# Kernel optimization log

Measured on AMD Instinct MI355X. Metric: run time of the kernel, lower is better.

The kernel has to match this reference:

```python
import jax, jax.numpy as jnp
import numpy as np

ALPHA = 0.2
WINDOW = 5
LAYER_CNN = 3
LAYER_OUT = 3
BIDAT = 4
B, N, M, CD, GD, NH, LD, PD = 32, 128, 1024, 128, 64, 4, 256, 40


def _gat(h, adj, W, a, concat):
    # e[b,i,j] = leaky_relu(a1 . Wh_i + a2 . Wh_j)  (decomposed repeat_interleave+cat+matmul)
    Wh = jnp.einsum('bnf,fg->bng', h, W)
    g = W.shape[1]
    e = jax.nn.leaky_relu(jnp.einsum('bng,g->bn', Wh, a[:g, 0])[:, :, None]
                          + jnp.einsum('bng,g->bn', Wh, a[g:, 0])[:, None, :], ALPHA)
    e = jnp.where(adj > 0, e, jnp.float32(-9e15))
    att = jax.nn.softmax(e, axis=2)
    hp = jnp.einsum('bnm,bmg->bng', att, Wh)
    return jax.nn.elu(hp) if concat else hp


def _mask_softmax(a, mask):
    a_exp = jnp.exp(a - jnp.max(a, -1, keepdims=True)) * mask
    return a_exp / (jnp.sum(a_exp, -1, keepdims=True) + 1e-6)


def reference(atoms_emb, adjacency, atoms_mask, amino_emb, amino_mask, fps, inv_Temp, Temp,
              bert_W, bert_b, gat_W, gat_a, gatout_W, gatout_a, Wcomp_W, Wcomp_b,
              prot_W, prot_b, conv_W, conv_b, Wprot_W, Wprot_b,
              U, tc2p_W, tc2p_b, tp2c_W, tp2c_b, bhc_W, bhc_b, bhp_W, bhp_b,
              battc_W, battc_b, battp_W, battp_b, combc_W, combc_b, combp_W, combp_b,
              Wout_W, Wout_b, out_W, out_b):
    # compound branch: bert projection 300 -> comp_dim, then multi-head GAT
    h = jnp.einsum('bnc,cd->bnd', atoms_emb, bert_W) + bert_b
    heads = jax.vmap(lambda W, a: _gat(h, adjacency, W, a, True))(gat_W, gat_a)  # [H,B,N,GD]
    multi = jnp.moveaxis(heads, 0, 2).reshape(h.shape[0], h.shape[1], -1)        # [B,N,H*GD]
    av = jax.nn.elu(_gat(multi, adjacency, gatout_W, gatout_a, False))
    av = jax.nn.leaky_relu(jnp.einsum('bnd,dl->bnl', av, Wcomp_W) + Wcomp_b, ALPHA)  # [B,N,LD]
    # protein branch: 1024 -> prot_dim, stacked 2D conv (1 channel), prot_dim -> latent
    pv = jnp.einsum('bmc,cd->bmd', amino_emb, prot_W) + prot_b  # [B,M,PD]
    x = pv[:, None, :, :]  # NCHW
    for i in range(LAYER_CNN):
        x = jax.nn.leaky_relu(
            jax.lax.conv_general_dilated(x, conv_W[i][None, None], (1, 1),
                                         [(WINDOW, WINDOW), (WINDOW, WINDOW)],
                                         dimension_numbers=('NCHW', 'OIHW', 'NCHW')) + conv_b[i], ALPHA)
    pv = jax.nn.leaky_relu(jnp.einsum('bmd,dl->bml', x[:, 0], Wprot_W) + Wprot_b, ALPHA)  # [B,M,LD]
    # bidirectional U-bilinear co-attention, BIDAT rounds
    cfs, pfs = [], []
    for i in range(BIDAT):
        A = jnp.tanh(jnp.einsum('bnl,lk,bmk->bnm', av, U[i], pv))
        A = A * atoms_mask[:, :, None] * amino_mask[:, None, :]
        atoms_trans = jnp.einsum('bnm,bml->bnl', A, jnp.tanh(jnp.einsum('bml,lk->bmk', pv, tp2c_W[i]) + tp2c_b[i]))
        amino_trans = jnp.einsum('bnm,bnl->bml', A, jnp.tanh(jnp.einsum('bnl,lk->bnk', av, tc2p_W[i]) + tc2p_b[i]))
        atoms_tmp = jnp.concatenate([jnp.tanh(jnp.einsum('bnl,lk->bnk', av, bhc_W[i]) + bhc_b[i]), atoms_trans], -1)
        amino_tmp = jnp.concatenate([jnp.tanh(jnp.einsum('bml,lk->bmk', pv, bhp_W[i]) + bhp_b[i]), amino_trans], -1)
        atoms_att = _mask_softmax(jnp.einsum('bnd,d->bn', atoms_tmp, battc_W[i]) + battc_b[i], atoms_mask)
        amino_att = _mask_softmax(jnp.einsum('bmd,d->bm', amino_tmp, battp_W[i]) + battp_b[i], amino_mask)
        cfs.append(jnp.sum(av * atoms_att[:, :, None], 1))
        pfs.append(jnp.sum(pv * amino_att[:, :, None], 1))
    cat_cf = jnp.concatenate(cfs, 1)  # [B, BIDAT*LD]
    cat_pf = jnp.concatenate(pfs, 1)
    cf_final = jnp.concatenate([cat_cf @ combc_W + combc_b, fps], 1)
    pf_final = cat_pf @ combp_W + combp_b
    v = jnp.concatenate([cf_final, pf_final, inv_Temp, Temp], 1)  # [B, 3*LD+2]
    for j in range(LAYER_OUT):
        v = jax.nn.leaky_relu(v @ Wout_W[j] + Wout_b[j], ALPHA)
    return v @ out_W + out_b  # [B,1]


def setup_inputs():
    ks = jax.random.split(jax.random.key(0), 64)
    def nrm(i, shape, s=0.1):
        return (jax.random.normal(ks[i], shape) * s).astype(jnp.float32)
    adjacency = jax.random.randint(ks[0], (B, N, N), 0, 2).astype(jnp.int32)
    adjacency = jnp.maximum(adjacency, jnp.eye(N, dtype=jnp.int32)[None])  # self-loops
    K = 2 * WINDOW + 1
    return dict(
        atoms_emb=nrm(1, (B, N, 300), 1.0),
        adjacency=adjacency,
        atoms_mask=jnp.ones((B, N), jnp.float32),
        amino_emb=nrm(2, (B, M, 1024), 1.0),
        amino_mask=jnp.ones((B, M), jnp.float32),
        fps=nrm(3, (B, LD), 1.0),
        inv_Temp=jax.random.uniform(ks[4], (B, 1), jnp.float32),
        Temp=jax.random.uniform(ks[5], (B, 1), jnp.float32),
        bert_W=nrm(6, (300, CD)), bert_b=nrm(7, (CD,)),
        gat_W=nrm(8, (NH, CD, GD)), gat_a=nrm(9, (NH, 2 * GD, 1)),
        gatout_W=nrm(10, (NH * GD, CD)), gatout_a=nrm(11, (2 * CD, 1)),
        Wcomp_W=nrm(12, (CD, LD)), Wcomp_b=nrm(13, (LD,)),
        prot_W=nrm(14, (1024, PD)), prot_b=nrm(15, (PD,)),
        conv_W=nrm(16, (LAYER_CNN, K, K)), conv_b=nrm(17, (LAYER_CNN,)),
        Wprot_W=nrm(18, (PD, LD)), Wprot_b=nrm(19, (LD,)),
        U=nrm(20, (BIDAT, LD, LD)),
        tc2p_W=nrm(21, (BIDAT, LD, LD)), tc2p_b=nrm(22, (BIDAT, LD)),
        tp2c_W=nrm(23, (BIDAT, LD, LD)), tp2c_b=nrm(24, (BIDAT, LD)),
        bhc_W=nrm(25, (BIDAT, LD, LD)), bhc_b=nrm(26, (BIDAT, LD)),
        bhp_W=nrm(27, (BIDAT, LD, LD)), bhp_b=nrm(28, (BIDAT, LD)),
        battc_W=nrm(29, (BIDAT, 2 * LD)), battc_b=nrm(30, (BIDAT,)),
        battp_W=nrm(31, (BIDAT, 2 * LD)), battp_b=nrm(32, (BIDAT,)),
        combc_W=nrm(33, (BIDAT * LD, LD)), combc_b=nrm(34, (LD,)),
        combp_W=nrm(35, (BIDAT * LD, LD)), combp_b=nrm(36, (LD,)),
        Wout_W=nrm(37, (LAYER_OUT, 3 * LD + 2, 3 * LD + 2)), Wout_b=nrm(38, (LAYER_OUT, 3 * LD + 2)),
        out_W=nrm(39, (3 * LD + 2, 1)), out_b=nrm(40, (1,)),
    )
```

## Files before the change

kernel.cpp:

```cpp
#include <hip/hip_runtime.h>
#include <math.h>

#define ALPHA_LR 0.2f

#define Bq  32
#define Nq  128
#define Mq  1024
#define CDq 128
#define GDq 64
#define NHq 4
#define LDq 256
#define PDq 40

typedef unsigned short ushort_t;
typedef __attribute__((ext_vector_type(8))) short bf16x8;
typedef __attribute__((ext_vector_type(4))) float f32x4;

__device__ __forceinline__ ushort_t f2bf(float f) {
    union { float f; unsigned u; } x; x.f = f;
    unsigned r = x.u + 0x7FFFu + ((x.u >> 16) & 1u);
    return (ushort_t)(r >> 16);
}
__device__ __forceinline__ float bf2f(ushort_t u) {
    union { unsigned u; float f; } x; x.u = ((unsigned)u) << 16;
    return x.f;
}
__device__ __forceinline__ float ftanh(float x) {
    float e = __expf(2.f * x);
    return 1.f - 2.f * __builtin_amdgcn_rcpf(e + 1.f);
}

template<int ACT, int MASKED, int HAS_BIAS, int NT, int AF32, int OUTBF>
__global__ __launch_bounds__(256) void mfma_nt_k(
    int M, int N, int K, int Nout,
    const void* __restrict__ Av, int lda, long long sA,
    const ushort_t* __restrict__ Bt, int ldb, long long sB,
    const float* __restrict__ bias, long long sBias,
    void* __restrict__ Cv, int ldc, long long sC,
    const float* __restrict__ maskR, long long sW2,
    const float* __restrict__ maskC)
{
    int z = blockIdx.z;
    Bt += (long long)z * sB;
    if (HAS_BIAS) bias += (long long)z * sBias;
    float* C = nullptr; ushort_t* Cb = nullptr;
    if (OUTBF) Cb = (ushort_t*)Cv + (long long)z * sC;
    else       C  = (float*)Cv + (long long)z * sC;

    int wave = threadIdx.x >> 6;
    int lane = threadIdx.x & 63;
    int lr = lane & 15;
    int kg = lane >> 4;
    int m0 = (blockIdx.x * 4 + wave) * 16;
    int n0 = blockIdx.y * (NT * 16);
    if (m0 >= M) return;

    f32x4 acc[NT];
    #pragma unroll
    for (int t = 0; t < NT; t++) acc[t] = (f32x4){0.f, 0.f, 0.f, 0.f};

    const ushort_t* Ab = nullptr;
    const float*    Af = nullptr;
    if (AF32) Af = (const float*)Av + (long long)z * sA + (long long)(m0 + lr) * lda + kg * 8;
    else      Ab = (const ushort_t*)Av + (long long)z * sA + (long long)(m0 + lr) * lda + kg * 8;
    const ushort_t* Bbase = Bt + (long long)(n0 + lr) * ldb + kg * 8;

    for (int k0 = 0; k0 < K; k0 += 32) {
        bf16x8 a;
        if (AF32) {
            float4 a0 = *(const float4*)(Af + k0);
            float4 a1 = *(const float4*)(Af + k0 + 4);
            a[0] = (short)f2bf(a0.x); a[1] = (short)f2bf(a0.y);
            a[2] = (short)f2bf(a0.z); a[3] = (short)f2bf(a0.w);
            a[4] = (short)f2bf(a1.x); a[5] = (short)f2bf(a1.y);
            a[6] = (short)f2bf(a1.z); a[7] = (short)f2bf(a1.w);
        } else {
            a = *(const bf16x8*)(Ab + k0);
        }
        #pragma unroll
        for (int t = 0; t < NT; t++) {
            bf16x8 b = *(const bf16x8*)(Bbase + (long long)t * 16 * ldb + k0);
            acc[t] = __builtin_amdgcn_mfma_f32_16x16x32_bf16(a, b, acc[t], 0, 0, 0);
        }
    }

    int row0 = m0 + kg * 4;
    #pragma unroll
    for (int t = 0; t < NT; t++) {
        int col = n0 + t * 16 + lr;
        if (col >= Nout) continue;
        float bv = HAS_BIAS ? bias[col] : 0.f;
        float mC = MASKED ? maskC[(long long)z * N + col] : 1.f;
        #pragma unroll
        for (int r = 0; r < 4; r++) {
            float v = acc[t][r] + bv;
            if (ACT == 1) v = v > 0.f ? v : ALPHA_LR * v;
            else if (ACT == 2) v = ftanh(v);
            if (MASKED) v *= maskR[(long long)z * M + row0 + r] * mC;
            if (OUTBF) Cb[(long long)(row0 + r) * ldc + col] = f2bf(v);
            else       C[(long long)(row0 + r) * ldc + col] = v;
        }
    }
}

__global__ __launch_bounds__(256) void pv0_k(
    const float* __restrict__ amino,
    const ushort_t* __restrict__ Bt,
    const float* __restrict__ bias,
    float* __restrict__ C)
{
    __shared__ float As[64][68];
    int tid = threadIdx.x;
    int wave = tid >> 6, lane = tid & 63;
    int lr = lane & 15, kg = lane >> 4;
    int m0 = blockIdx.x * 64;

    f32x4 acc[3];
    #pragma unroll
    for (int t = 0; t < 3; t++) acc[t] = (f32x4){0.f, 0.f, 0.f, 0.f};

    int srow = tid >> 2;
    int scol = (tid & 3) * 16;
    const float* srcbase = amino + (long long)(m0 + srow) * 1024 + scol;

    for (int k0 = 0; k0 < 1024; k0 += 64) {
        float4 v0 = *(const float4*)(srcbase + k0);
        float4 v1 = *(const float4*)(srcbase + k0 + 4);
        float4 v2 = *(const float4*)(srcbase + k0 + 8);
        float4 v3 = *(const float4*)(srcbase + k0 + 12);
        *(float4*)&As[srow][scol]      = v0;
        *(float4*)&As[srow][scol + 4]  = v1;
        *(float4*)&As[srow][scol + 8]  = v2;
        *(float4*)&As[srow][scol + 12] = v3;
        __syncthreads();
        #pragma unroll
        for (int ks = 0; ks < 2; ks++) {
            const float* ap = &As[wave * 16 + lr][ks * 32 + kg * 8];
            bf16x8 a;
            #pragma unroll
            for (int j = 0; j < 8; j++) a[j] = (short)f2bf(ap[j]);
            #pragma unroll
            for (int t = 0; t < 3; t++) {
                bf16x8 bfr = *(const bf16x8*)(Bt + (long long)(t * 16 + lr) * 1024 + k0 + ks * 32 + kg * 8);
                acc[t] = __builtin_amdgcn_mfma_f32_16x16x32_bf16(a, bfr, acc[t], 0, 0, 0);
            }
        }
        __syncthreads();
    }
    int row0 = m0 + wave * 16 + kg * 4;
    #pragma unroll
    for (int t = 0; t < 3; t++) {
        int col = t * 16 + lr;
        if (col >= PDq) continue;
        float bv = bias[col];
        #pragma unroll
        for (int r = 0; r < 4; r++)
            C[(long long)(row0 + r) * PDq + col] = acc[t][r] + bv;
    }
}

__global__ __launch_bounds__(256) void mfma_reduceF_k(
    int M,
    const ushort_t* __restrict__ A,
    const ushort_t* __restrict__ W8,
    const float* __restrict__ bias8,
    const float* __restrict__ w28,
    float* __restrict__ C)
{
    int z = blockIdx.z;
    const ushort_t* W = W8 + (long long)z * 65536;
    const float* bias = bias8 + z * 256;
    const float* w2   = w28 + z * 256;
    float* Cz = C + (long long)z * M;

    __shared__ ushort_t Bs[64 * 256];

    int tid = threadIdx.x;
    int wave = tid >> 6, lane = tid & 63;
    int lr = lane & 15, kg = lane >> 4;
    int m0 = blockIdx.x * 128 + wave * 16;

    const ushort_t* Ab0 = A + (long long)(m0 + lr) * 256 + kg * 8;
    const ushort_t* Ab1 = Ab0 + 64 * 256;
    bf16x8 areg0[8], areg1[8];
    #pragma unroll
    for (int kb = 0; kb < 8; kb++) {
        areg0[kb] = *(const bf16x8*)(Ab0 + kb * 32);
        areg1[kb] = *(const bf16x8*)(Ab1 + kb * 32);
    }

    float rs0[4] = {0.f, 0.f, 0.f, 0.f};
    float rs1[4] = {0.f, 0.f, 0.f, 0.f};

    for (int ph = 0; ph < 4; ph++) {
        int n0 = ph * 64;
        #pragma unroll
        for (int step = 0; step < 8; step++) {
            int g = step * 256 + tid;
            int row = g >> 5, slot = g & 31;
            uint4 v = *(const uint4*)(W + (long long)(n0 + row) * 256 + slot * 8);
            int dst = row * 512 + ((slot * 16) ^ ((row & 31) << 4));
            *(uint4*)((char*)Bs + dst) = v;
        }
        __syncthreads();

        {
            f32x4 acc[4];
            #pragma unroll
            for (int t = 0; t < 4; t++) acc[t] = (f32x4){0.f, 0.f, 0.f, 0.f};
            #pragma unroll
            for (int kb = 0; kb < 8; kb++) {
                #pragma unroll
                for (int t = 0; t < 4; t++) {
                    int rowl = t * 16 + lr;
                    int colb = (kg * 16 + kb * 64) ^ ((rowl & 31) << 4);
                    bf16x8 b = *(const bf16x8*)((char*)Bs + rowl * 512 + colb);
                    acc[t] = __builtin_amdgcn_mfma_f32_16x16x32_bf16(areg0[kb], b, acc[t], 0, 0, 0);
                }
            }
            #pragma unroll
            for (int t = 0; t < 4; t++) {
                int col = n0 + t * 16 + lr;
                float bv = bias[col], wv = w2[col];
                #pragma unroll
                for (int r = 0; r < 4; r++)
                    rs0[r] += ftanh(acc[t][r] + bv) * wv;
            }
        }
        {
            f32x4 acc[4];
            #pragma unroll
            for (int t = 0; t < 4; t++) acc[t] = (f32x4){0.f, 0.f, 0.f, 0.f};
            #pragma unroll
            for (int kb = 0; kb < 8; kb++) {
                #pragma unroll
                for (int t = 0; t < 4; t++) {
                    int rowl = t * 16 + lr;
                    int colb = (kg * 16 + kb * 64) ^ ((rowl & 31) << 4);
                    bf16x8 b = *(const bf16x8*)((char*)Bs + rowl * 512 + colb);
                    acc[t] = __builtin_amdgcn_mfma_f32_16x16x32_bf16(areg1[kb], b, acc[t], 0, 0, 0);
                }
            }
            #pragma unroll
            for (int t = 0; t < 4; t++) {
                int col = n0 + t * 16 + lr;
                float bv = bias[col], wv = w2[col];
                #pragma unroll
                for (int r = 0; r < 4; r++)
                    rs1[r] += ftanh(acc[t][r] + bv) * wv;
            }
        }
        __syncthreads();
    }

    #pragma unroll
    for (int r = 0; r < 4; r++) {
        rs0[r] += __shfl_xor(rs0[r], 1, 64);
        rs0[r] += __shfl_xor(rs0[r], 2, 64);
        rs0[r] += __shfl_xor(rs0[r], 4, 64);
        rs0[r] += __shfl_xor(rs0[r], 8, 64);
        rs1[r] += __shfl_xor(rs1[r], 1, 64);
        rs1[r] += __shfl_xor(rs1[r], 2, 64);
        rs1[r] += __shfl_xor(rs1[r], 4, 64);
        rs1[r] += __shfl_xor(rs1[r], 8, 64);
    }
    if (lr == 0) {
        int row0 = m0 + kg * 4;
        #pragma unroll
        for (int r = 0; r < 4; r++) {
            Cz[row0 + r] = rs0[r];
            Cz[row0 + 64 + r] = rs1[r];
        }
    }
}

__global__ __launch_bounds__(256) void pack8_k(
    const float* __restrict__ b1, const float* __restrict__ b2,
    const float* __restrict__ w1, int w1Off,
    const float* __restrict__ w2v, int w2Off,
    float* __restrict__ bias8, float* __restrict__ w28)
{
    int j = blockIdx.x * 256 + threadIdx.x;
    int slot = j >> 8, c = j & 255;
    bias8[j] = slot < 4 ? b1[slot * 256 + c] : b2[(slot - 4) * 256 + c];
    w28[j]   = slot < 4 ? w1[slot * 512 + w1Off + c] : w2v[(slot - 4) * 512 + w2Off + c];
}

__global__ __launch_bounds__(256) void bidat_fused_k(
    const ushort_t* __restrict__ avU_all,
    const ushort_t* __restrict__ pv_bf,
    const float* __restrict__ rbuf_all,
    const float* __restrict__ qbuf_all,
    const float* __restrict__ atoms_mask,
    const float* __restrict__ amino_mask,
    float* __restrict__ scoreCp,
    float* __restrict__ csump)
{
    int z = blockIdx.z;
    int i = z >> 5, b = z & 31;
    int gx = blockIdx.x;
    int gy = blockIdx.y;
    int wave = threadIdx.x >> 6;
    int lane = threadIdx.x & 63;
    int lr = lane & 15, kg = lane >> 4;

    int n0 = gx * 64 + wave * 16;
    const ushort_t* Ab = avU_all + ((long long)i * 4096 + (long long)b * 128 + n0 + lr) * 256 + kg * 8;
    bf16x8 areg[8];
    #pragma unroll
    for (int kb = 0; kb < 8; kb++) areg[kb] = *(const bf16x8*)(Ab + kb * 32);

    const float* rI = rbuf_all + (long long)i * 32768 + (long long)b * 1024;
    const float* qI = qbuf_all + (long long)i * 4096 + (long long)b * 128;
    const float* mR = atoms_mask + (long long)b * 128;
    const float* mC = amino_mask + (long long)b * 1024;

    float mRn[4], qn[4];
    #pragma unroll
    for (int r = 0; r < 4; r++) {
        int n = n0 + kg * 4 + r;
        mRn[r] = mR[n];
        qn[r]  = qI[n];
    }

    float sc[4] = {0.f, 0.f, 0.f, 0.f};
    __shared__ float cl[4][64];

    for (int mt = 0; mt < 4; mt++) {
        int m0 = (gy * 4 + mt) * 64;
        const ushort_t* Bb = pv_bf + ((long long)b * 1024 + m0 + lr) * 256 + kg * 8;

        f32x4 acc[4];
        #pragma unroll
        for (int t = 0; t < 4; t++) acc[t] = (f32x4){0.f, 0.f, 0.f, 0.f};
        #pragma unroll
        for (int kb = 0; kb < 8; kb++) {
            #pragma unroll
            for (int t = 0; t < 4; t++) {
                bf16x8 bfr = *(const bf16x8*)(Bb + (long long)t * 16 * 256 + kb * 32);
                acc[t] = __builtin_amdgcn_mfma_f32_16x16x32_bf16(areg[kb], bfr, acc[t], 0, 0, 0);
            }
        }

        float cs[4] = {0.f, 0.f, 0.f, 0.f};
        #pragma unroll
        for (int t = 0; t < 4; t++) {
            int m = m0 + t * 16 + lr;
            float mc = mC[m];
            float rv = rI[m];
            #pragma unroll
            for (int r = 0; r < 4; r++) {
                float a = ftanh(acc[t][r]) * mRn[r] * mc;
                sc[r] += a * rv;
                cs[t] += a * qn[r];
            }
        }
        #pragma unroll
        for (int t = 0; t < 4; t++) {
            cs[t] += __shfl_xor(cs[t], 16, 64);
            cs[t] += __shfl_xor(cs[t], 32, 64);
        }
        __syncthreads();
        if (kg == 0) {
            #pragma unroll
            for (int t = 0; t < 4; t++) cl[wave][t * 16 + lr] = cs[t];
        }
        __syncthreads();
        if (threadIdx.x < 64) {
            float s = cl[0][threadIdx.x] + cl[1][threadIdx.x]
                    + cl[2][threadIdx.x] + cl[3][threadIdx.x];
            csump[((long long)z * 2 + gx) * 1024 + m0 + threadIdx.x] = s;
        }
    }

    #pragma unroll
    for (int r = 0; r < 4; r++) {
        sc[r] += __shfl_xor(sc[r], 1, 64);
        sc[r] += __shfl_xor(sc[r], 2, 64);
        sc[r] += __shfl_xor(sc[r], 4, 64);
        sc[r] += __shfl_xor(sc[r], 8, 64);
    }
    if (lr == 0) {
        #pragma unroll
        for (int r = 0; r < 4; r++) {
            int n = gx * 64 + wave * 16 + kg * 4 + r;
            scoreCp[((long long)z * 4 + gy) * 128 + n] = sc[r];
        }
    }
}

__global__ __launch_bounds__(128) void finishC_sm_k(
    const float* __restrict__ scoreCp, const float* __restrict__ hbdot_all,
    const float* __restrict__ battc_b, const float* __restrict__ mask,
    float* __restrict__ scoreC_all)
{
    int z = blockIdx.x;
    int i = z >> 5, b = z & 31;
    int n = threadIdx.x;
    __shared__ float red[128];
    float s = 0.f;
    #pragma unroll
    for (int gy = 0; gy < 4; gy++)
        s += scoreCp[((long long)z * 4 + gy) * 128 + n];
    s += hbdot_all[(long long)i * 4096 + b * 128 + n] + battc_b[i];
    red[n] = s; __syncthreads();
    for (int off = 64; off > 0; off >>= 1) {
        if (n < off) red[n] = fmaxf(red[n], red[n + off]);
        __syncthreads();
    }
    float mx = red[0];
    __syncthreads();
    float e = __expf(s - mx) * mask[(long long)b * 128 + n];
    red[n] = e; __syncthreads();
    for (int off = 64; off > 0; off >>= 1) {
        if (n < off) red[n] += red[n + off];
        __syncthreads();
    }
    float inv = 1.0f / (red[0] + 1e-6f);
    scoreC_all[(long long)z * 128 + n] = e * inv;
}

__global__ __launch_bounds__(256) void finishP_sm_k(
    const float* __restrict__ csump, const float* __restrict__ hpbdot_all,
    const float* __restrict__ battp_b, const float* __restrict__ mask,
    float* __restrict__ scoreP_all)
{
    int z = blockIdx.x;
    int i = z >> 5, b = z & 31;
    int t = threadIdx.x;
    __shared__ float red[256];
    float vals[4];
    float mx = -1e30f;
    #pragma unroll
    for (int j = 0; j < 4; j++) {
        int m = j * 256 + t;
        float s = csump[((long long)z * 2 + 0) * 1024 + m]
                + csump[((long long)z * 2 + 1) * 1024 + m]
                + hpbdot_all[(long long)i * 32768 + (long long)b * 1024 + m]
                + battp_b[i];
        vals[j] = s;
        mx = fmaxf(mx, s);
    }
    red[t] = mx; __syncthreads();
    for (int off = 128; off > 0; off >>= 1) {
        if (t < off) red[t] = fmaxf(red[t], red[t + off]);
        __syncthreads();
    }
    mx = red[0];
    __syncthreads();
    float sum = 0.f;
    #pragma unroll
    for (int j = 0; j < 4; j++) {
        float e = __expf(vals[j] - mx) * mask[(long long)b * 1024 + j * 256 + t];
        vals[j] = e; sum += e;
    }
    red[t] = sum; __syncthreads();
    for (int off = 128; off > 0; off >>= 1) {
        if (t < off) red[t] += red[t + off];
        __syncthreads();
    }
    float inv = 1.0f / (red[0] + 1e-6f);
    #pragma unroll
    for (int j = 0; j < 4; j++)
        scoreP_all[(long long)z * 1024 + j * 256 + t] = vals[j] * inv;
}

__global__ __launch_bounds__(256) void cvtpad_bf16_k(
    const float* __restrict__ in, ushort_t* __restrict__ out,
    int rows, int Ksrc, int Kdst)
{
    long long idx = (long long)blockIdx.x * 256 + threadIdx.x;
    long long total = (long long)rows * Kdst;
    if (idx >= total) return;
    int r = (int)(idx / Kdst), k = (int)(idx % Kdst);
    out[idx] = (k < Ksrc) ? f2bf(in[(long long)r * Ksrc + k]) : (ushort_t)0;
}

struct WtEnt {
    const float* W; ushort_t* Wt;
    int K, Nsrc, Npad, Kp, zcnt, blkStart;
};
struct WtTab { WtEnt e[11]; };

__global__ __launch_bounds__(256) void wtcvtAll_k(WtTab tab)
{
    int blk = blockIdx.x;
    int ei = 0;
    #pragma unroll
    for (int i = 1; i < 11; i++) if (blk >= tab.e[i].blkStart) ei = i;
    WtEnt E = tab.e[ei];
    long long perZ = (long long)E.Npad * E.Kp;
    long long lidx = (long long)(blk - E.blkStart) * 256 + threadIdx.x;
    if (lidx >= perZ * E.zcnt) return;
    int z = (int)(lidx / perZ);
    long long idx = lidx % perZ;
    int n = (int)(idx / E.Kp), k = (int)(idx % E.Kp);
    const float* Wz = E.W + (long long)z * E.K * E.Nsrc;
    ushort_t* Oz = E.Wt + (long long)z * perZ;
    float v = (k < E.K && n < E.Nsrc) ? Wz[(long long)k * E.Nsrc + n] : 0.f;
    Oz[idx] = f2bf(v);
}

__global__ __launch_bounds__(128) void gat_e_k(
    const float* __restrict__ Wh, int ldWh, int GD,
    const float* __restrict__ a, int aStride,
    float* __restrict__ esrc, float* __restrict__ edst, int rows)
{
    int row = blockIdx.x;
    int k = blockIdx.y;
    int g = threadIdx.x;
    float ws = 0.f, wd = 0.f;
    if (g < GD) {
        float wv = Wh[(long long)row * ldWh + k * GD + g];
        ws = wv * a[k * aStride + g];
        wd = wv * a[k * aStride + GD + g];
    }
    __shared__ float sb[2][128];
    sb[0][threadIdx.x] = ws; sb[1][threadIdx.x] = wd;
    __syncthreads();
    for (int off = 64; off > 0; off >>= 1) {
        if (threadIdx.x < off) {
            sb[0][threadIdx.x] += sb[0][threadIdx.x + off];
            sb[1][threadIdx.x] += sb[1][threadIdx.x + off];
        }
        __syncthreads();
    }
    if (threadIdx.x == 0) {
        esrc[(long long)k * rows + row] = sb[0][0];
        edst[(long long)k * rows + row] = sb[1][0];
    }
}

template<int GD>
__global__ __launch_bounds__(256) void gat_attn2_k(
    const float* __restrict__ Wh, int ldWh,
    const int* __restrict__ adj,
    const float* __restrict__ esrc, const float* __restrict__ edst,
    ushort_t* __restrict__ outp, int ldOut)
{
    int row = blockIdx.x;
    int k = blockIdx.y;
    int rows = gridDim.x;
    int b = row >> 7, n = row & 127;
    int tid = threadIdx.x;

    __shared__ float att[128];
    __shared__ float red[128];
    __shared__ float sred[256];

    if (tid < 128) {
        float e = esrc[(long long)k * rows + row] + edst[(long long)k * rows + b * 128 + tid];
        e = e > 0.f ? e : ALPHA_LR * e;
        if (adj[(long long)b * 16384 + n * 128 + tid] <= 0) e = -9.0e15f;
        att[tid] = e;
        red[tid] = e;
    }
    __syncthreads();
    for (int off = 64; off > 0; off >>= 1) {
        if (tid < off) red[tid] = fmaxf(red[tid], red[tid + off]);
        __syncthreads();
    }
    float mx = red[0];
    __syncthreads();
    if (tid < 128) {
        float ex = __expf(att[tid] - mx);
        att[tid] = ex;
        red[tid] = ex;
    }
    __syncthreads();
    for (int off = 64; off > 0; off >>= 1) {
        if (tid < off) red[tid] += red[tid + off];
        __syncthreads();
    }
    float inv = 1.0f / red[0];
    __syncthreads();

    constexpr int SPLIT = 256 / GD;
    constexpr int CH = 128 / SPLIT;
    int g = tid % GD;
    int part = tid / GD;
    const float* Whb = Wh + (long long)(b * 128) * ldWh + k * GD + g;
    float s = 0.f;
    int mm0 = part * CH;
    for (int mm = mm0; mm < mm0 + CH; mm++)
        s += att[mm] * Whb[(long long)mm * ldWh];
    sred[part * GD + g] = s;
    __syncthreads();
    if (part == 0) {
        float tot = s;
        #pragma unroll
        for (int p = 1; p < SPLIT; p++) tot += sred[p * GD + g];
        tot *= inv;
        tot = tot > 0.f ? tot : expm1f(tot);
        outp[(long long)row * ldOut + k * GD + g] = f2bf(tot);
    }
}

__global__ __launch_bounds__(256) void conv3_k(
    const float* __restrict__ x,
    const float* __restrict__ Wc,
    const float* __restrict__ bc,
    ushort_t* __restrict__ y)
{
    __shared__ float wsh[3][121];
    __shared__ float A[94][50];
    __shared__ float Bv[84][50];
    __shared__ float Cv[74][50];

    int tid = threadIdx.x;
    int b = blockIdx.y;
    int m0 = blockIdx.x * 64;

    for (int i = tid; i < 363; i += 256) wsh[i / 121][i % 121] = Wc[i];
    const float* xb = x + (long long)b * Mq * PDq;
    for (int idx = tid; idx < 94 * 50; idx += 256) {
        int row = idx / 50, col = idx % 50;
        int gm = m0 - 15 + row, d = col - 5;
        float v = 0.f;
        if (d >= 0 && d < PDq && gm >= 0 && gm < Mq)
            v = xb[(long long)gm * PDq + d];
        A[row][col] = v;
    }
    __syncthreads();

    {
        float b0 = bc[0];
        for (int idx = tid; idx < 84 * 50; idx += 256) {
            int row = idx / 50, col = idx % 50;
            float s = 0.f;
            if (col >= 5 && col < 45) {
                int d = col - 5;
                #pragma unroll
                for (int i = 0; i < 11; i++)
                    #pragma unroll
                    for (int j = 0; j < 11; j++)
                        s += A[row + i][d + j] * wsh[0][i * 11 + j];
                s += b0;
                s = s > 0.f ? s : ALPHA_LR * s;
            }
            Bv[row][col] = s;
        }
    }
    __syncthreads();

    {
        float b1 = bc[1];
        for (int idx = tid; idx < 74 * 50; idx += 256) {
            int row = idx / 50, col = idx % 50;
            float s = 0.f;
            if (col >= 5 && col < 45) {
                int d = col - 5;
                #pragma unroll
                for (int i = 0; i < 11; i++)
                    #pragma unroll
                    for (int j = 0; j < 11; j++)
                        s += Bv[row + i][d + j] * wsh[1][i * 11 + j];
                s += b1;
                s = s > 0.f ? s : ALPHA_LR * s;
            }
            Cv[row][col] = s;
        }
    }
    __syncthreads();

    {
        float b2 = bc[2];
        for (int idx = tid; idx < 64 * 64; idx += 256) {
            int row = idx / 64, d = idx % 64;
            long long o = ((long long)b * Mq + m0 + row) * 64 + d;
            if (d >= PDq) { y[o] = 0; continue; }
            float s = 0.f;
            #pragma unroll
            for (int i = 0; i < 11; i++)
                #pragma unroll
                for (int j = 0; j < 11; j++)
                    s += Cv[row + i][d + j] * wsh[2][i * 11 + j];
            s += b2;
            s = s > 0.f ? s : ALPHA_LR * s;
            y[o] = f2bf(s);
        }
    }
}

__global__ __launch_bounds__(256) void wsum1B4_k(
    const ushort_t* __restrict__ feat, const float* __restrict__ att_all,
    float* __restrict__ partial, int L)
{
    int b = blockIdx.x, c = blockIdx.y, l = threadIdx.x;
    int chunk = L / 16;
    const ushort_t* fb = feat + (long long)b * L * LDq;
    const float* a0 = att_all + ((long long)0 * Bq + b) * L;
    const float* a1 = att_all + ((long long)1 * Bq + b) * L;
    const float* a2 = att_all + ((long long)2 * Bq + b) * L;
    const float* a3 = att_all + ((long long)3 * Bq + b) * L;
    float s0 = 0.f, s1 = 0.f, s2 = 0.f, s3 = 0.f;
    int r0 = c * chunk, r1 = r0 + chunk;
    for (int r = r0; r < r1; r++) {
        float f = bf2f(fb[(long long)r * LDq + l]);
        s0 += f * a0[r]; s1 += f * a1[r];
        s2 += f * a2[r]; s3 += f * a3[r];
    }
    partial[(((long long)0 * Bq + b) * 16 + c) * LDq + l] = s0;
    partial[(((long long)1 * Bq + b) * 16 + c) * LDq + l] = s1;
    partial[(((long long)2 * Bq + b) * 16 + c) * LDq + l] = s2;
    partial[(((long long)3 * Bq + b) * 16 + c) * LDq + l] = s3;
}

__global__ __launch_bounds__(256) void wsum2B_k(
    const float* __restrict__ partial, float* __restrict__ out)
{
    int b = blockIdx.x, i = blockIdx.y, l = threadIdx.x;
    float s = 0.f;
    #pragma unroll
    for (int c = 0; c < 16; c++)
        s += partial[(((long long)i * Bq + b) * 16 + c) * LDq + l];
    out[(long long)b * 4 * LDq + i * LDq + l] = s;
}

template<int ACT>
__global__ __launch_bounds__(256) void headlin_k(
    const float* __restrict__ vin, int ldv, int VD,
    const float* __restrict__ W, int ldw,
    const float* __restrict__ bias,
    float* __restrict__ vout, int ldo, int OD, int colBase)
{
    int b = blockIdx.x;
    int c = threadIdx.x & 63;
    int s = threadIdx.x >> 6;
    int col = blockIdx.y * 64 + c;

    __shared__ float vs[1024];
    for (int i = threadIdx.x; i < VD; i += 256) vs[i] = vin[(long long)b * ldv + i];
    __syncthreads();

    float sum = 0.f;
    if (col < OD) {
        int k0 = (VD * s) >> 2, k1 = (VD * (s + 1)) >> 2;
        #pragma unroll 4
        for (int k = k0; k < k1; k++)
            sum += vs[k] * W[(long long)k * ldw + col];
    }
    __shared__ float red[4][64];
    red[s][c] = sum;
    __syncthreads();
    if (s == 0 && col < OD) {
        float t = red[0][c] + red[1][c] + red[2][c] + red[3][c] + bias[col];
        if (ACT == 1) t = t > 0.f ? t : ALPHA_LR * t;
        vout[(long long)b * ldo + colBase + col] = t;
    }
}

__global__ __launch_bounds__(256) void vfill_k(
    const float* __restrict__ fps, const float* __restrict__ invT,
    const float* __restrict__ T, float* __restrict__ v)
{
    int b = blockIdx.x, t = threadIdx.x;
    v[(long long)b * 770 + 256 + t] = fps[(long long)b * 256 + t];
    if (t == 0) {
        v[(long long)b * 770 + 768] = invT[b];
        v[(long long)b * 770 + 769] = T[b];
    }
}

__global__ __launch_bounds__(256) void final_k(
    const float* __restrict__ v, const float* __restrict__ W,
    const float* __restrict__ bptr, float* __restrict__ out)
{
    int b = blockIdx.x, t = threadIdx.x;
    float s = 0.f;
    for (int i = t; i < 770; i += 256) s += v[(long long)b * 770 + i] * W[i];
    __shared__ float red[256];
    red[t] = s; __syncthreads();
    for (int off = 128; off > 0; off >>= 1) {
        if (t < off) red[t] += red[t + off];
        __syncthreads();
    }
    if (t == 0) out[b] = red[0] + bptr[0];
}

extern "C" void kernel_launch(void* const* d_in, const int* in_sizes, int n_in,
                              void* d_out, int out_size, void* d_ws, size_t ws_size,
                              hipStream_t stream)
{
    const float* atoms_emb = (const float*)d_in[0];
    const int*   adjacency = (const int*)d_in[1];
    const float* atoms_mask= (const float*)d_in[2];
    const float* amino_emb = (const float*)d_in[3];
    const float* amino_mask= (const float*)d_in[4];
    const float* fps       = (const float*)d_in[5];
    const float* inv_Temp  = (const float*)d_in[6];
    const float* Temp      = (const float*)d_in[7];
    const float* bert_W    = (const float*)d_in[8];
    const float* bert_b    = (const float*)d_in[9];
    const float* gat_W     = (const float*)d_in[10];
    const float* gat_a     = (const float*)d_in[11];
    const float* gatout_W  = (const float*)d_in[12];
    const float* gatout_a  = (const float*)d_in[13];
    const float* Wcomp_W   = (const float*)d_in[14];
    const float* Wcomp_b   = (const float*)d_in[15];
    const float* prot_W    = (const float*)d_in[16];
    const float* prot_b    = (const float*)d_in[17];
    const float* conv_W    = (const float*)d_in[18];
    const float* conv_b    = (const float*)d_in[19];
    const float* Wprot_W   = (const float*)d_in[20];
    const float* Wprot_b   = (const float*)d_in[21];
    const float* U         = (const float*)d_in[22];
    const float* tc2p_W    = (const float*)d_in[23];
    const float* tc2p_b    = (const float*)d_in[24];
    const float* tp2c_W    = (const float*)d_in[25];
    const float* tp2c_b    = (const float*)d_in[26];
    const float* bhc_W     = (const float*)d_in[27];
    const float* bhc_b     = (const float*)d_in[28];
    const float* bhp_W     = (const float*)d_in[29];
    const float* bhp_b     = (const float*)d_in[30];
    const float* battc_W   = (const float*)d_in[31];
    const float* battc_b   = (const float*)d_in[32];
    const float* battp_W   = (const float*)d_in[33];
    const float* battp_b   = (const float*)d_in[34];
    const float* combc_W   = (const float*)d_in[35];
    const float* combc_b   = (const float*)d_in[36];
    const float* combp_W   = (const float*)d_in[37];
    const float* combp_b   = (const float*)d_in[38];
    const float* Wout_W    = (const float*)d_in[39];
    const float* Wout_b    = (const float*)d_in[40];
    const float* out_W     = (const float*)d_in[41];
    const float* out_b     = (const float*)d_in[42];
    float* out = (float*)d_out;

    float* w = (float*)d_ws;
    float* av    = w; w += (long long)Bq*Nq*LDq;
    float* pv    = w; w += (long long)Bq*Mq*LDq;
    float* sx    = w; w += (long long)Bq*Mq*LDq;
    float* pool  = w; w += (long long)Bq*Nq*Mq;
    float* bufU  = w; w += (long long)Bq*Nq*LDq;
    float* bufTC = w; w += (long long)Bq*Nq*LDq;
    float* esrc  = w; w += (long long)NHq*Bq*Nq;
    float* edst  = w; w += (long long)NHq*Bq*Nq;
    float* scoreC= w; w += (long long)Bq*Nq;
    float* scoreP= w; w += (long long)Bq*Mq;
    float* rbuf  = w; w += (long long)Bq*Mq;
    float* qbuf  = w; w += (long long)Bq*Nq;
    float* csum  = w; w += (long long)Bq*Mq;
    float* cf    = w; w += (long long)Bq*4*LDq;
    float* pf    = w; w += (long long)Bq*4*LDq;
    float* v1    = w; w += (long long)Bq*770;
    float* v2    = w; w += (long long)Bq*770;
    ushort_t* pv_bf  = (ushort_t*)w; w += (long long)Bq*Mq*LDq/2;
    ushort_t* av_bf  = (ushort_t*)w; w += (long long)Bq*Nq*LDq/2;
    ushort_t* avU_bf = (ushort_t*)w; w += (long long)Bq*Nq*LDq/2;
    ushort_t* Ut_bf     = (ushort_t*)w; w += (long long)4*LDq*LDq/2;
    ushort_t* protWt_bf = (ushort_t*)w; w += (long long)48*1024/2;
    ushort_t* bertWt_bf = (ushort_t*)w; w += (long long)128*320/2;
    ushort_t* gatWt_bf  = (ushort_t*)w; w += (long long)4*64*128/2;
    ushort_t* gatoutWt_bf=(ushort_t*)w; w += (long long)128*256/2;
    ushort_t* WcompT_bf = (ushort_t*)w; w += (long long)256*128/2;
    ushort_t* WprotT_bf = (ushort_t*)w; w += (long long)256*64/2;
    ushort_t* wP_bf     = (ushort_t*)w; w += (long long)8*256*256/2;
    ushort_t* wA_bf     = (ushort_t*)w; w += (long long)8*256*256/2;

    int rowsA = Bq * Nq;
    int rowsP = Bq * Mq;

    float* h     = sx;
    float* WhAll = h + (long long)rowsA*CDq;
    float* multi = WhAll + (long long)rowsA*NHq*GDq;
    float* Wh2   = multi + (long long)rowsA*NHq*GDq;
    float* avp   = Wh2 + (long long)rowsA*CDq;
    float* c0    = avp + (long long)rowsA*CDq;
    float* c1    = c0 + (long long)rowsP*PDq;

    ushort_t* atoms_bf = (ushort_t*)pool;
    ushort_t* h_bf     = atoms_bf + (long long)rowsA*320;
    ushort_t* multi_bf = h_bf + (long long)rowsA*128;
    ushort_t* avp_bf   = multi_bf + (long long)rowsA*256;
    ushort_t* c1_bf    = avp_bf + (long long)rowsA*128;

    float*    rbuf_all   = sx;
    float*    hpbdot_all = rbuf_all   + (long long)4*rowsP;
    float*    qbuf_all   = hpbdot_all + (long long)4*rowsP;
    float*    hbdot_all  = qbuf_all   + (long long)4*rowsA;
    float*    bufU_all   = hbdot_all  + (long long)4*rowsA;
    ushort_t* avU_all_bf = (ushort_t*)(bufU_all + (long long)4*rowsA*LDq);

    float* scoreCp    = pool;
    float* csump      = scoreCp + 65536;
    float* scoreC_all = csump + 262144;
    float* scoreP_all = scoreC_all + 16384;

    float* wpart = bufTC;

    float* bias8P = rbuf;
    float* w28P   = rbuf + 2048;
    float* bias8A = rbuf + 4096;
    float* w28A   = rbuf + 6144;

    WtTab tab;
    int blk = 0;
    auto setent = [&](int i, const float* W, ushort_t* Wt,
                      int K, int Nsrc, int Npad, int Kp, int zc) {
        tab.e[i].W = W; tab.e[i].Wt = Wt;
        tab.e[i].K = K; tab.e[i].Nsrc = Nsrc; tab.e[i].Npad = Npad;
        tab.e[i].Kp = Kp; tab.e[i].zcnt = zc; tab.e[i].blkStart = blk;
        blk += (int)(((long long)zc * Npad * Kp + 255) / 256);
    };
    setent(0,  U,        Ut_bf,       256, 256, 256, 256, 4);
    setent(1,  prot_W,   protWt_bf,   1024, 40, 48, 1024, 1);
    setent(2,  bert_W,   bertWt_bf,   300, 128, 128, 320, 1);
    setent(3,  gat_W,    gatWt_bf,    128, 64,  64,  128, 4);
    setent(4,  gatout_W, gatoutWt_bf, 256, 128, 128, 256, 1);
    setent(5,  Wcomp_W,  WcompT_bf,   128, 256, 256, 128, 1);
    setent(6,  Wprot_W,  WprotT_bf,   40,  256, 256, 64,  1);
    setent(7,  tp2c_W,   wP_bf,              256, 256, 256, 256, 4);
    setent(8,  bhp_W,    wP_bf + 4*65536,    256, 256, 256, 256, 4);
    setent(9,  tc2p_W,   wA_bf,              256, 256, 256, 256, 4);
    setent(10, bhc_W,    wA_bf + 4*65536,    256, 256, 256, 256, 4);
    wtcvtAll_k<<<blk, 256, 0, stream>>>(tab);
    pack8_k<<<8, 256, 0, stream>>>(tp2c_b, bhp_b, battc_W, 256, battp_W, 0, bias8P, w28P);
    pack8_k<<<8, 256, 0, stream>>>(tc2p_b, bhc_b, battp_W, 256, battc_W, 0, bias8A, w28A);

    cvtpad_bf16_k<<<(int)(((long long)rowsA*320 + 255)/256), 256, 0, stream>>>(
        atoms_emb, atoms_bf, rowsA, 300, 320);
    mfma_nt_k<0, 0, 1, 2, 0, 1><<<dim3(rowsA/64, 4, 1), 256, 0, stream>>>(
        rowsA, CDq, 320, CDq, (const void*)atoms_bf, 320, 0,
        bertWt_bf, 320, 0, bert_b, 0, (void*)h_bf, CDq, 0, nullptr, 0, nullptr);

    mfma_nt_k<0, 0, 0, 4, 0, 0><<<dim3(rowsA/64, 1, 4), 256, 0, stream>>>(
        rowsA, GDq, CDq, GDq, (const void*)h_bf, CDq, 0,
        gatWt_bf, CDq, (long long)GDq*CDq,
        nullptr, 0, (void*)WhAll, NHq*GDq, GDq, nullptr, 0, nullptr);

    gat_e_k<<<dim3(rowsA, NHq), 128, 0, stream>>>(WhAll, NHq*GDq, GDq, gat_a, 2*GDq,
                                                  esrc, edst, rowsA);
    gat_attn2_k<64><<<dim3(rowsA, NHq), 256, 0, stream>>>(WhAll, NHq*GDq, adjacency,
                                                          esrc, edst, multi_bf, NHq*GDq);

    mfma_nt_k<0, 0, 0, 2, 0, 0><<<dim3(rowsA/64, 4, 1), 256, 0, stream>>>(
        rowsA, CDq, 256, CDq, (const void*)multi_bf, 256, 0,
        gatoutWt_bf, 256, 0, nullptr, 0, (void*)Wh2, CDq, 0, nullptr, 0, nullptr);
    gat_e_k<<<dim3(rowsA, 1), 128, 0, stream>>>(Wh2, CDq, CDq, gatout_a, 2*CDq,
                                                esrc, edst, rowsA);
    gat_attn2_k<128><<<dim3(rowsA, 1), 256, 0, stream>>>(Wh2, CDq, adjacency,
                                                         esrc, edst, avp_bf, CDq);

    mfma_nt_k<1, 0, 1, 4, 0, 1><<<dim3(rowsA/64, 4, 1), 256, 0, stream>>>(
        rowsA, LDq, CDq, LDq, (const void*)avp_bf, CDq, 0,
        WcompT_bf, CDq, 0, Wcomp_b, 0, (void*)av_bf, LDq, 0, nullptr, 0, nullptr);

    pv0_k<<<rowsP/64, 256, 0, stream>>>(amino_emb, protWt_bf, prot_b, c0);

    conv3_k<<<dim3(Mq/64, Bq), 256, 0, stream>>>(c0, conv_W, conv_b, c1_bf);

    mfma_nt_k<1, 0, 1, 4, 0, 1><<<dim3(rowsP/64, 4, 1), 256, 0, stream>>>(
        rowsP, LDq, 64, LDq, (const void*)c1_bf, 64, 0,
        WprotT_bf, 64, 0, Wprot_b, 0, (void*)pv_bf, LDq, 0, nullptr, 0, nullptr);

    mfma_reduceF_k<<<dim3(rowsP/128, 1, 8), 256, 0, stream>>>(
        rowsP, pv_bf, wP_bf, bias8P, w28P, rbuf_all);
    mfma_reduceF_k<<<dim3(rowsA/128, 1, 8), 256, 0, stream>>>(
        rowsA, av_bf, wA_bf, bias8A, w28A, qbuf_all);
    mfma_nt_k<0, 0, 0, 4, 0, 1><<<dim3(rowsA/64, 4, 4), 256, 0, stream>>>(
        rowsA, LDq, LDq, LDq, (const void*)av_bf, LDq, 0,
        Ut_bf, LDq, (long long)LDq*LDq,
        nullptr, 0, (void*)avU_all_bf, LDq, (long long)rowsA*LDq,
        nullptr, 0, nullptr);

    bidat_fused_k<<<dim3(2, 4, 128), 256, 0, stream>>>(
        avU_all_bf, pv_bf, rbuf_all, qbuf_all,
        atoms_mask, amino_mask, scoreCp, csump);
    finishC_sm_k<<<128, 128, 0, stream>>>(scoreCp, hbdot_all, battc_b,
                                          atoms_mask, scoreC_all);
    finishP_sm_k<<<128, 256, 0, stream>>>(csump, hpbdot_all, battp_b,
                                          amino_mask, scoreP_all);

    wsum1B4_k<<<dim3(Bq, 16), 256, 0, stream>>>(av_bf, scoreC_all, wpart, Nq);
    wsum2B_k<<<dim3(Bq, 4), 256, 0, stream>>>(wpart, cf);
    wsum1B4_k<<<dim3(Bq, 16), 256, 0, stream>>>(pv_bf, scoreP_all, wpart, Mq);
    wsum2B_k<<<dim3(Bq, 4), 256, 0, stream>>>(wpart, pf);

    headlin_k<0><<<dim3(Bq, 4), 256, 0, stream>>>(cf, 4*LDq, 4*LDq,
        combc_W, LDq, combc_b, v1, 770, LDq, 0);
    headlin_k<0><<<dim3(Bq, 4), 256, 0, stream>>>(pf, 4*LDq, 4*LDq,
        combp_W, LDq, combp_b, v1, 770, LDq, 512);
    vfill_k<<<Bq, 256, 0, stream>>>(fps, inv_Temp, Temp, v1);

    headlin_k<1><<<dim3(Bq, 13), 256, 0, stream>>>(v1, 770, 770,
        Wout_W + 0ll*770*770, 770, Wout_b + 0*770, v2, 770, 770, 0);
    headlin_k<1><<<dim3(Bq, 13), 256, 0, stream>>>(v2, 770, 770,
        Wout_W + 1ll*770*770, 770, Wout_b + 1*770, v1, 770, 770, 0);
    headlin_k<1><<<dim3(Bq, 13), 256, 0, stream>>>(v1, 770, 770,
        Wout_W + 2ll*770*770, 770, Wout_b + 2*770, v2, 770, 770, 0);

    final_k<<<Bq, 256, 0, stream>>>(v2, out_W, out_b, out);

    (void)in_sizes; (void)n_in; (void)out_size; (void)ws_size;
    (void)av; (void)pv; (void)bufU; (void)avU_bf; (void)qbuf; (void)csum;
    (void)scoreC; (void)scoreP; (void)h; (void)multi; (void)avp; (void)bufU_all; (void)c1;
}
```

Before: 512.5 us.

## Widen reduceF tiles to 256 rows and fuse partial-sum reduction into head linear

mfma_reduceF_k now processes four 64-row A tiles per block instead of two, so each staged weight tile in LDS is reused across twice as many rows and the grid is halved. Separately, the wsum2B reduction kernels are removed and the 16-way partial sum is folded into a new headlinP_k that loads the partials straight into shared memory before the combine linear layer. This drops two launches and an intermediate buffer round trip. It also uses a separate partial buffer for the protein path so both wsum1 launches can run before the heads. The costs are higher register pressure (32 bf16x8 A fragments per thread) and fewer blocks for the MFMA kernel.

```diff
diff --git a/kernel.cpp b/kernel.cpp
--- a/kernel.cpp
+++ b/kernel.cpp
@@ -178,19 +178,18 @@
     int tid = threadIdx.x;
     int wave = tid >> 6, lane = tid & 63;
     int lr = lane & 15, kg = lane >> 4;
-    int m0 = blockIdx.x * 128 + wave * 16;
-
-    const ushort_t* Ab0 = A + (long long)(m0 + lr) * 256 + kg * 8;
-    const ushort_t* Ab1 = Ab0 + 64 * 256;
-    bf16x8 areg0[8], areg1[8];
-    #pragma unroll
-    for (int kb = 0; kb < 8; kb++) {
-        areg0[kb] = *(const bf16x8*)(Ab0 + kb * 32);
-        areg1[kb] = *(const bf16x8*)(Ab1 + kb * 32);
-    }
-
-    float rs0[4] = {0.f, 0.f, 0.f, 0.f};
-    float rs1[4] = {0.f, 0.f, 0.f, 0.f};
+    int m0 = blockIdx.x * 256 + wave * 16;
+
+    bf16x8 areg[4][8];
+    #pragma unroll
+    for (int t4 = 0; t4 < 4; t4++) {
+        const ushort_t* Ab = A + (long long)(m0 + t4 * 64 + lr) * 256 + kg * 8;
+        #pragma unroll
+        for (int kb = 0; kb < 8; kb++)
+            areg[t4][kb] = *(const bf16x8*)(Ab + kb * 32);
+    }
+
+    float rs[4][4] = {};
 
     for (int ph = 0; ph < 4; ph++) {
         int n0 = ph * 64;
@@ -204,7 +203,8 @@
         }
         __syncthreads();
 
-        {
+        #pragma unroll
+        for (int t4 = 0; t4 < 4; t4++) {
             f32x4 acc[4];
             #pragma unroll
             for (int t = 0; t < 4; t++) acc[t] = (f32x4){0.f, 0.f, 0.f, 0.f};
@@ -215,7 +215,7 @@
                     int rowl = t * 16 + lr;
                     int colb = (kg * 16 + kb * 64) ^ ((rowl & 31) << 4);
                     bf16x8 b = *(const bf16x8*)((char*)Bs + rowl * 512 + colb);
-                    acc[t] = __builtin_amdgcn_mfma_f32_16x16x32_bf16(areg0[kb], b, acc[t], 0, 0, 0);
+                    acc[t] = __builtin_amdgcn_mfma_f32_16x16x32_bf16(areg[t4][kb], b, acc[t], 0, 0, 0);
                 }
             }
             #pragma unroll
@@ -224,53 +224,29 @@
                 float bv = bias[col], wv = w2[col];
                 #pragma unroll
                 for (int r = 0; r < 4; r++)
-                    rs0[r] += ftanh(acc[t][r] + bv) * wv;
+                    rs[t4][r] += ftanh(acc[t][r] + bv) * wv;
             }
         }
-        {
-            f32x4 acc[4];
-            #pragma unroll
-            for (int t = 0; t < 4; t++) acc[t] = (f32x4){0.f, 0.f, 0.f, 0.f};
-            #pragma unroll
-            for (int kb = 0; kb < 8; kb++) {
-                #pragma unroll
-                for (int t = 0; t < 4; t++) {
-                    int rowl = t * 16 + lr;
-                    int colb = (kg * 16 + kb * 64) ^ ((rowl & 31) << 4);
-                    bf16x8 b = *(const bf16x8*)((char*)Bs + rowl * 512 + colb);
-                    acc[t] = __builtin_amdgcn_mfma_f32_16x16x32_bf16(areg1[kb], b, acc[t], 0, 0, 0);
-                }
-            }
-            #pragma unroll
-            for (int t = 0; t < 4; t++) {
-                int col = n0 + t * 16 + lr;
-                float bv = bias[col], wv = w2[col];
-                #pragma unroll
-                for (int r = 0; r < 4; r++)
-                    rs1[r] += ftanh(acc[t][r] + bv) * wv;
-            }
-        }
-        __syncthreads();
-    }
-
-    #pragma unroll
-    for (int r = 0; r < 4; r++) {
-        rs0[r] += __shfl_xor(rs0[r], 1, 64);
-        rs0[r] += __shfl_xor(rs0[r], 2, 64);
-        rs0[r] += __shfl_xor(rs0[r], 4, 64);
-        rs0[r] += __shfl_xor(rs0[r], 8, 64);
-        rs1[r] += __shfl_xor(rs1[r], 1, 64);
-        rs1[r] += __shfl_xor(rs1[r], 2, 64);
-        rs1[r] += __shfl_xor(rs1[r], 4, 64);
-        rs1[r] += __shfl_xor(rs1[r], 8, 64);
+        __syncthreads();
+    }
+
+    #pragma unroll
+    for (int t4 = 0; t4 < 4; t4++) {
+        #pragma unroll
+        for (int r = 0; r < 4; r++) {
+            rs[t4][r] += __shfl_xor(rs[t4][r], 1, 64);
+            rs[t4][r] += __shfl_xor(rs[t4][r], 2, 64);
+            rs[t4][r] += __shfl_xor(rs[t4][r], 4, 64);
+            rs[t4][r] += __shfl_xor(rs[t4][r], 8, 64);
+        }
     }
     if (lr == 0) {
         int row0 = m0 + kg * 4;
         #pragma unroll
-        for (int r = 0; r < 4; r++) {
-            Cz[row0 + r] = rs0[r];
-            Cz[row0 + 64 + r] = rs1[r];
-        }
+        for (int t4 = 0; t4 < 4; t4++)
+            #pragma unroll
+            for (int r = 0; r < 4; r++)
+                Cz[row0 + t4 * 64 + r] = rs[t4][r];
     }
 }
 
@@ -706,15 +682,42 @@
     partial[(((long long)3 * Bq + b) * 16 + c) * LDq + l] = s3;
 }
 
-__global__ __launch_bounds__(256) void wsum2B_k(
-    const float* __restrict__ partial, float* __restrict__ out)
-{
-    int b = blockIdx.x, i = blockIdx.y, l = threadIdx.x;
-    float s = 0.f;
-    #pragma unroll
-    for (int c = 0; c < 16; c++)
-        s += partial[(((long long)i * Bq + b) * 16 + c) * LDq + l];
-    out[(long long)b * 4 * LDq + i * LDq + l] = s;
+__global__ __launch_bounds__(256) void headlinP_k(
+    const float* __restrict__ partial,
+    const float* __restrict__ W, int ldw,
+    const float* __restrict__ bias,
+    float* __restrict__ vout, int ldo, int OD, int colBase)
+{
+    int b = blockIdx.x;
+    int c = threadIdx.x & 63;
+    int s = threadIdx.x >> 6;
+    int col = blockIdx.y * 64 + c;
+
+    __shared__ float vs[1024];
+    for (int j = threadIdx.x; j < 1024; j += 256) {
+        int i = j >> 8, l = j & 255;
+        const float* pbase = partial + (((long long)i * Bq + b) * 16) * LDq + l;
+        float acc = 0.f;
+        #pragma unroll
+        for (int cc = 0; cc < 16; cc++) acc += pbase[cc * LDq];
+        vs[j] = acc;
+    }
+    __syncthreads();
+
+    float sum = 0.f;
+    if (col < OD) {
+        int k0 = 256 * s, k1 = 256 * (s + 1);
+        #pragma unroll 4
+        for (int k = k0; k < k1; k++)
+            sum += vs[k] * W[(long long)k * ldw + col];
+    }
+    __shared__ float red[4][64];
+    red[s][c] = sum;
+    __syncthreads();
+    if (s == 0 && col < OD) {
+        float t = red[0][c] + red[1][c] + red[2][c] + red[3][c] + bias[col];
+        vout[(long long)b * ldo + colBase + col] = t;
+    }
 }
 
 template<int ACT>
@@ -887,7 +890,8 @@
     float* scoreC_all = csump + 262144;
     float* scoreP_all = scoreC_all + 16384;
 
-    float* wpart = bufTC;
+    float* wpartC = bufTC;
+    float* wpartP = bufU;
 
     float* bias8P = rbuf;
     float* w28P   = rbuf + 2048;
@@ -954,9 +958,9 @@
         rowsP, LDq, 64, LDq, (const void*)c1_bf, 64, 0,
         WprotT_bf, 64, 0, Wprot_b, 0, (void*)pv_bf, LDq, 0, nullptr, 0, nullptr);
 
-    mfma_reduceF_k<<<dim3(rowsP/128, 1, 8), 256, 0, stream>>>(
+    mfma_reduceF_k<<<dim3(rowsP/256, 1, 8), 256, 0, stream>>>(
         rowsP, pv_bf, wP_bf, bias8P, w28P, rbuf_all);
-    mfma_reduceF_k<<<dim3(rowsA/128, 1, 8), 256, 0, stream>>>(
+    mfma_reduceF_k<<<dim3(rowsA/256, 1, 8), 256, 0, stream>>>(
         rowsA, av_bf, wA_bf, bias8A, w28A, qbuf_all);
     mfma_nt_k<0, 0, 0, 4, 0, 1><<<dim3(rowsA/64, 4, 4), 256, 0, stream>>>(
         rowsA, LDq, LDq, LDq, (const void*)av_bf, LDq, 0,
@@ -972,14 +976,12 @@
     finishP_sm_k<<<128, 256, 0, stream>>>(csump, hpbdot_all, battp_b,
                                           amino_mask, scoreP_all);
 
-    wsum1B4_k<<<dim3(Bq, 16), 256, 0, stream>>>(av_bf, scoreC_all, wpart, Nq);
-    wsum2B_k<<<dim3(Bq, 4), 256, 0, stream>>>(wpart, cf);
-    wsum1B4_k<<<dim3(Bq, 16), 256, 0, stream>>>(pv_bf, scoreP_all, wpart, Mq);
-    wsum2B_k<<<dim3(Bq, 4), 256, 0, stream>>>(wpart, pf);
-
-    headlin_k<0><<<dim3(Bq, 4), 256, 0, stream>>>(cf, 4*LDq, 4*LDq,
+    wsum1B4_k<<<dim3(Bq, 16), 256, 0, stream>>>(av_bf, scoreC_all, wpartC, Nq);
+    wsum1B4_k<<<dim3(Bq, 16), 256, 0, stream>>>(pv_bf, scoreP_all, wpartP, Mq);
+
+    headlinP_k<<<dim3(Bq, 4), 256, 0, stream>>>(wpartC,
         combc_W, LDq, combc_b, v1, 770, LDq, 0);
-    headlin_k<0><<<dim3(Bq, 4), 256, 0, stream>>>(pf, 4*LDq, 4*LDq,
+    headlinP_k<<<dim3(Bq, 4), 256, 0, stream>>>(wpartP,
         combp_W, LDq, combp_b, v1, 770, LDq, 512);
     vfill_k<<<Bq, 256, 0, stream>>>(fps, inv_Temp, Temp, v1);
 
@@ -993,6 +995,7 @@
     final_k<<<Bq, 256, 0, stream>>>(v2, out_W, out_b, out);
 
     (void)in_sizes; (void)n_in; (void)out_size; (void)ws_size;
-    (void)av; (void)pv; (void)bufU; (void)avU_bf; (void)qbuf; (void)csum;
-    (void)scoreC; (void)scoreP; (void)h; (void)multi; (void)avp; (void)bufU_all; (void)c1;
-}
+    (void)av; (void)pv; (void)avU_bf; (void)qbuf; (void)csum;
+    (void)scoreC; (void)scoreP; (void)h; (void)multi; (void)avp;
+    (void)bufU_all; (void)c1; (void)cf; (void)pf;
+}
```

New measurement: 528.6 us. 1.03x slower.
